# Optimization experiments

Measured on AMD Instinct MI355X. Metric: run time of the kernel, lower is better.

The kernel has to match this reference:

```python
import jax, jax.numpy as jnp
import numpy as np
from jax import lax

C = 256
K = 3
KK = K * K
PAD = 1


def conv2d(x, w, b, pad):
    # x: [B,Cin,H,W], w: [Cout,Cin,kh,kw]
    y = lax.conv_general_dilated(x, w, (1, 1), [(pad, pad), (pad, pad)],
                                 dimension_numbers=("NCHW", "OIHW", "NCHW"))
    return y + b[None, :, None, None]


def _bilinear_gather(x, ys, xs):
    # x: [B,C,H,W]; ys, xs: [B,KK,H,W] float sample coords (pixel space).
    # Zero padding outside the image (torchvision deform_conv2d semantics).
    B, Cc, H, W = x.shape
    y0 = jnp.floor(ys)
    x0 = jnp.floor(xs)
    fy = ys - y0
    fx = xs - x0
    xf = x.reshape(B, Cc, H * W)

    def gather_b(xb, ib):
        return jnp.take(xb, ib, axis=1)  # [C, KK*H*W]

    out = jnp.zeros((B, Cc, KK, H, W), dtype=x.dtype)
    corners = [
        (y0, x0, (1 - fy) * (1 - fx)),
        (y0, x0 + 1, (1 - fy) * fx),
        (y0 + 1, x0, fy * (1 - fx)),
        (y0 + 1, x0 + 1, fy * fx),
    ]
    for yi, xi, wgt in corners:
        valid = (yi >= 0) & (yi < H) & (xi >= 0) & (xi < W)
        yc = jnp.clip(yi, 0, H - 1).astype(jnp.int32)
        xc = jnp.clip(xi, 0, W - 1).astype(jnp.int32)
        idx = (yc * W + xc).reshape(B, -1)  # [B, KK*H*W]
        g = jax.vmap(gather_b)(xf, idx).reshape(B, Cc, KK, H, W)
        out = out + g * (wgt * valid.astype(x.dtype))[:, None]
    return out


def deform_conv2d(x, offset, weight):
    # x: [B,C,H,W]; offset: [B, 2*KK, H, W] with layout (k, (dy, dx));
    # weight: [Cout, Cin, K, K]; stride 1, padding 1, no mask/bias.
    B, Cin, H, W = x.shape
    off = offset.reshape(B, KK, 2, H, W)
    dy = off[:, :, 0]  # [B,KK,H,W]
    dx = off[:, :, 1]
    ky = (jnp.arange(KK, dtype=x.dtype) // K) - PAD  # kernel row offsets
    kx = (jnp.arange(KK, dtype=x.dtype) % K) - PAD
    ys = dy + jnp.arange(H, dtype=x.dtype)[None, None, :, None] + ky[None, :, None, None]
    xs = dx + jnp.arange(W, dtype=x.dtype)[None, None, None, :] + kx[None, :, None, None]
    sampled = _bilinear_gather(x, ys, xs)  # [B,Cin,KK,H,W]
    Cout = weight.shape[0]
    return jnp.einsum("bckhw,ock->bohw", sampled, weight.reshape(Cout, Cin, KK))


def setup_inputs() -> dict:
    key = jax.random.key(0)
    ks = jax.random.split(key, 12)
    B, H, W = 2, 128, 128
    s = 0.05
    inp = {
        "ft_1": jax.random.normal(ks[0], (B, C, H, W), jnp.float32),
        "ft_2": jax.random.normal(ks[1], (B, C, H, W), jnp.float32),
        "ft_3": jax.random.normal(ks[2], (B, C, H, W), jnp.float32),
        "w1": jax.random.normal(ks[3], (256, 3 * C, 3, 3), jnp.float32) * s,
        "b1": jnp.zeros((256,), jnp.float32),
        "w2": jax.random.normal(ks[4], (256, 256, 3, 3), jnp.float32) * s,
        "b2": jnp.zeros((256,), jnp.float32),
        # last offset conv is zero-init in the original; use small random
        # values so the deformable sampling path is actually exercised
        "w3": jax.random.normal(ks[5], (2 * KK * 2, 256, 3, 3), jnp.float32) * 0.01,
        "b3": jax.random.normal(ks[6], (2 * KK * 2,), jnp.float32) * 0.01,
        "w_dcn2": jax.random.normal(ks[7], (C, C, 3, 3), jnp.float32) * s,
        "w_dcn3": jax.random.normal(ks[8], (C, C, 3, 3), jnp.float32) * s,
        "w_fuse": jax.random.normal(ks[9], (C, 3 * C, 1, 1), jnp.float32) * s,
        "b_fuse": jnp.zeros((C,), jnp.float32),
    }
    return inp


def reference(ft_1, ft_2, ft_3, w1, b1, w2, b2, w3, b3,
              w_dcn2, w_dcn3, w_fuse, b_fuse):
    combined = jnp.concatenate([ft_1, ft_2, ft_3], axis=1)  # [B,3C,H,W]
    h = jax.nn.relu(conv2d(combined, w1, b1, 1))
    h = jax.nn.relu(conv2d(h, w2, b2, 1))
    offsets_all = conv2d(h, w3, b3, 1)  # [B, 36, H, W]
    half = offsets_all.shape[1] // 2
    off_2 = offsets_all[:, :half]
    off_3 = offsets_all[:, half:]
    ft_2_aligned = deform_conv2d(ft_2, off_2, w_dcn2)
    ft_3_aligned = deform_conv2d(ft_3, off_3, w_dcn3)
    fused_raw = jnp.concatenate([ft_1, ft_2_aligned, ft_3_aligned], axis=1)
    return conv2d(fused_raw, w_fuse, b_fuse, 0)
```

## Files before the change

kernel.cpp:

```cpp
#include <hip/hip_runtime.h>
#include <stdint.h>

#define H_ 128
#define W_ 128
#define HW_ 16384
#define B_ 2
#define XP_ 130

typedef __attribute__((ext_vector_type(4))) float f32x4;
typedef _Float16 half_t;
typedef __attribute__((ext_vector_type(8))) _Float16 h8v;
typedef __attribute__((ext_vector_type(4))) _Float16 h4v;

__device__ __forceinline__ f32x4 MFMA(h8v a, h8v b, f32x4 c) {
  return __builtin_amdgcn_mfma_f32_16x16x32_f16(a, b, c, 0, 0, 0);
}
__device__ __forceinline__ f32x4 zero4() {
  f32x4 z; z[0] = 0.f; z[1] = 0.f; z[2] = 0.f; z[3] = 0.f; return z;
}
__device__ __forceinline__ int swz(int r, int c8) {
  return r * 64 + ((c8 ^ (r & 7)) << 3);
}

template <int N>
__device__ __forceinline__ void s_wait_vmcnt() {
  asm volatile("s_waitcnt vmcnt(%0)" ::"n"(N) : "memory");
}

typedef const __attribute__((address_space(1))) uint32_t glb_u32;
typedef __attribute__((address_space(3))) uint32_t lds_u32;
__device__ __forceinline__ void gl_lds16(const half_t* g, half_t* l) {
  __builtin_amdgcn_global_load_lds((glb_u32*)(uintptr_t)g,
                                   (lds_u32*)(uint32_t)(uintptr_t)l, 16, 0, 0);
}

__global__ __launch_bounds__(256) void zeropad(half_t* __restrict__ buf, int C) {
  int nc = C >> 3;
  int total = B_ * 516 * nc;
  int idx = blockIdx.x * 256 + threadIdx.x;
  if (idx >= total) return;
  int c8 = idx % nc;
  int p = idx / nc;
  int b = p / 516, i = p % 516;
  int y, x;
  if (i < 130) { y = 0; x = i; }
  else if (i < 260) { y = 129; x = i - 130; }
  else if (i < 388) { y = i - 260 + 1; x = 0; }
  else { y = i - 388 + 1; x = 129; }
  h8v z;
#pragma unroll
  for (int j = 0; j < 8; ++j) z[j] = (half_t)0.f;
  *(h8v*)(buf + ((size_t)(b * XP_ + y) * XP_ + x) * C + c8 * 8) = z;
}

__global__ __launch_bounds__(256) void pack_x(
    const float* __restrict__ f1, const float* __restrict__ f2,
    const float* __restrict__ f3, half_t* __restrict__ xcat) {
  __shared__ float tile[64][65];
  int bid = blockIdx.x;
  int t = bid % 24, by = bid / 24;
  int b = by >> 7, y = by & 127;
  int s = t / 8, t2 = t % 8;
  int x0 = (t2 & 1) * 64, c0 = (t2 >> 1) * 64;
  const float* f = (s == 0) ? f1 : ((s == 1) ? f2 : f3);
  int tid = threadIdx.x;
  int rx = tid & 63, rc = tid >> 6;
  const float* srcp = f + ((size_t)(b * 256 + c0)) * HW_ + (size_t)y * W_ + x0;
#pragma unroll
  for (int i = 0; i < 16; ++i) {
    int c = rc + i * 4;
    tile[c][rx] = srcp[(size_t)c * HW_ + rx];
  }
  __syncthreads();
#pragma unroll
  for (int it = 0; it < 2; ++it) {
    int task = tid + it * 256;
    int x = task & 63, c8 = task >> 6;
    h8v v;
#pragma unroll
    for (int j = 0; j < 8; ++j) v[j] = (half_t)tile[c8 * 8 + j][x];
    size_t pix = (size_t)(b * XP_ + y + 1) * XP_ + x0 + x + 1;
    *(h8v*)(xcat + pix * 768 + s * 256 + c0 + c8 * 8) = v;
  }
}

__global__ __launch_bounds__(256) void wtrans_swz(
    const float* __restrict__ w, half_t* __restrict__ wt,
    int CO, int CI) {
  int CS = CI >> 6;
  int idx = blockIdx.x * 256 + threadIdx.x;
  int e = idx & 8191, tile = idx >> 13;
  int task = e >> 3, j = e & 7;
  int r = task >> 3, c8 = (task & 7) ^ (r & 7);
  int tpb = 9 * CS;
  int coblk = tile / tpb, within = tile - coblk * tpb;
  int dx = within % 3, q = within / 3;
  int cs = q % CS, g = q / CS;
  int t = g * 3 + dx;
  int co = coblk * 128 + r;
  int ci = cs * 64 + c8 * 8 + j;
  float v = (co < CO) ? w[((size_t)co * CI + ci) * 9 + t] : 0.f;
  wt[idx] = (half_t)v;
}

__global__ __launch_bounds__(256) void wtrans_swz256(
    const float* __restrict__ w, half_t* __restrict__ wt) {
  int idx = blockIdx.x * 256 + threadIdx.x;
  int e = idx & 16383, tile = idx >> 14;
  int task = e >> 3, j = e & 7;
  int r = task >> 3, c8 = (task & 7) ^ (r & 7);
  int cs = tile & 3, t = tile >> 2;
  int ci = cs * 64 + c8 * 8 + j;
  wt[idx] = (half_t)w[((size_t)r * 256 + ci) * 9 + t];
}

__global__ __launch_bounds__(256) void fuse_wswz(
    const float* __restrict__ w, half_t* __restrict__ wt) {
  int idx = blockIdx.x * 256 + threadIdx.x;
  int e = idx & 8191, tile = idx >> 13;
  int task = e >> 3, j = e & 7;
  int r = task >> 3, c8 = (task & 7) ^ (r & 7);
  int cs = tile % 12, coblk = tile / 12;
  int co = coblk * 128 + r;
  int ci = cs * 64 + c8 * 8 + j;
  wt[idx] = (half_t)w[(size_t)co * 768 + ci];
}

template <int CIN, bool RELU, bool FP32OUT>
__global__ __launch_bounds__(256) void conv3x3(
    const half_t* __restrict__ in, const half_t* __restrict__ wt,
    const float* __restrict__ bias, half_t* __restrict__ outb,
    float* __restrict__ outf, int COUT) {
  constexpr int CS = CIN / 64;
  constexpr int NGI = 3 * CS;
  __shared__ __align__(16) half_t wl[2][8192];
  __shared__ __align__(16) half_t al[2][8704];
  int tid = threadIdx.x;
  int by = blockIdx.x;
  int b = by >> 7, y = by & 127;
  int co0 = blockIdx.y * 128;
  int w = tid >> 6, l = tid & 63, lr = l & 15, lg = l >> 4;
  int wr = (w >> 1) * 64, wc = (w & 1) * 64;
  f32x4 acc[4][4];
#pragma unroll
  for (int i = 0; i < 4; ++i)
#pragma unroll
    for (int j = 0; j < 4; ++j) acc[i][j] = zero4();

  const half_t* wbase = wt + (size_t)blockIdx.y * (9 * CS) * 8192;

  int ldsoff[4], aoff[4], ldsoff4, aoff4;
#pragma unroll
  for (int it = 0; it < 4; ++it) {
    int task = tid + it * 256;
    ldsoff[it] = task * 8;
    int r = task >> 3, c8 = (task & 7) ^ (r & 7);
    aoff[it] = r * CIN + c8 * 8;
  }
  {
    int task = 1024 + tid;
    ldsoff4 = task * 8;
    int r = task >> 3, c8 = (task & 7) ^ (r & 7);
    aoff4 = r * CIN + c8 * 8;
  }

  auto stage_w = [&](int s, int buf) {
    const half_t* wp = wbase + (size_t)s * 8192;
#pragma unroll
    for (int it = 0; it < 4; ++it)
      gl_lds16(wp + ldsoff[it], &wl[buf][ldsoff[it]]);
  };
  auto stage_a = [&](int gi, int buf) {
    int g = gi / CS, cs = gi - g * CS;
    const half_t* ap = in + ((size_t)(b * XP_ + y + g) * XP_) * CIN + cs * 64;
    if (tid < 64) gl_lds16(ap + aoff4, &al[buf][ldsoff4]);
#pragma unroll
    for (int it = 0; it < 4; ++it)
      gl_lds16(ap + aoff[it], &al[buf][ldsoff[it]]);
  };
  auto compute = [&](int dx, int wbuf, int abuf) {
    const half_t* wb = wl[wbuf];
    const half_t* ab = al[abuf];
    h8v af[4][2], bf[4][2];
#pragma unroll
    for (int cg = 0; cg < 4; ++cg)
#pragma unroll
      for (int kc = 0; kc < 2; ++kc)
        af[cg][kc] = *(const h8v*)(wb + swz(wr + 16 * cg + lr, 4 * kc + lg));
#pragma unroll
    for (int pg = 0; pg < 4; ++pg)
#pragma unroll
      for (int kc = 0; kc < 2; ++kc)
        bf[pg][kc] = *(const h8v*)(ab + swz(wc + 16 * pg + lr + dx, 4 * kc + lg));
    __builtin_amdgcn_s_setprio(1);
#pragma unroll
    for (int cg = 0; cg < 4; ++cg)
#pragma unroll
      for (int pg = 0; pg < 4; ++pg) {
        acc[cg][pg] = MFMA(af[cg][0], bf[pg][0], acc[cg][pg]);
        acc[cg][pg] = MFMA(af[cg][1], bf[pg][1], acc[cg][pg]);
      }
    __builtin_amdgcn_s_setprio(0);
  };

  stage_w(0, 0);
  stage_a(0, 0);
  for (int gi = 0; gi < NGI; ++gi) {
    int abuf = gi & 1;
    int s0 = 3 * gi;
    stage_w(s0 + 1, (s0 + 1) & 1);
    s_wait_vmcnt<4>();
    __builtin_amdgcn_s_barrier();
    compute(0, s0 & 1, abuf);
    __builtin_amdgcn_s_barrier();
    stage_w(s0 + 2, s0 & 1);
    s_wait_vmcnt<4>();
    __builtin_amdgcn_s_barrier();
    compute(1, (s0 + 1) & 1, abuf);
    __builtin_amdgcn_s_barrier();
    if (gi + 1 < NGI) {
      stage_w(s0 + 3, (s0 + 3) & 1);
      stage_a(gi + 1, abuf ^ 1);
      s_wait_vmcnt<8>();
    } else {
      s_wait_vmcnt<0>();
    }
    __builtin_amdgcn_s_barrier();
    compute(2, s0 & 1, abuf);
    __builtin_amdgcn_s_barrier();
  }
#pragma unroll
  for (int cg = 0; cg < 4; ++cg) {
    int co = co0 + wr + 16 * cg + 4 * lg;
    if (FP32OUT && co >= COUT) continue;
    f32x4 bv = *(const f32x4*)(bias + co);
#pragma unroll
    for (int pg = 0; pg < 4; ++pg) {
      int px = wc + 16 * pg + lr;
      f32x4 v = acc[cg][pg];
#pragma unroll
      for (int r = 0; r < 4; ++r) {
        v[r] += bv[r];
        if (RELU) v[r] = fmaxf(v[r], 0.f);
      }
      if (FP32OUT) {
        size_t pix = (size_t)(b * H_ + y) * W_ + px;
        *(f32x4*)(outf + pix * COUT + co) = v;
      } else {
        size_t pix = (size_t)(b * XP_ + y + 1) * XP_ + px + 1;
        h4v pv;
#pragma unroll
        for (int r = 0; r < 4; ++r) pv[r] = (half_t)v[r];
        *(h4v*)(outb + pix * 256 + co) = pv;
      }
    }
  }
}

__global__ __launch_bounds__(512) void dcn(
    const half_t* __restrict__ xcat, int cbase,
    const float* __restrict__ off, int obase,
    const half_t* __restrict__ wt, half_t* __restrict__ outb) {
  __shared__ __align__(16) half_t wl[2][16384];
  __shared__ __align__(16) half_t al[2][8192];
  __shared__ int caddr[2][128][4];
  __shared__ float cwt[2][128][4];
  int tid = threadIdx.x;
  int bx = blockIdx.x;
  int by = ((bx & 7) << 5) | (bx >> 3);
  int b = by >> 7, y = by & 127;
  int w = tid >> 6, l = tid & 63, lr = l & 15, lg = l >> 4;
  int wr = (w >> 1) * 64, wc = (w & 1) * 64;
  size_t rowpix = (size_t)(b * H_ + y) * W_;
  f32x4 acc[4][4];
#pragma unroll
  for (int i = 0; i < 4; ++i)
#pragma unroll
    for (int j = 0; j < 4; ++j) acc[i][j] = zero4();

  auto coeffs = [&](int t) {
    if (tid < 128) {
      int px = tid;
      const float* op = off + (rowpix + px) * 36 + obase + 2 * t;
      float dy = op[0], dx = op[1];
      float ysf = (float)(y + (t / 3) - 1) + dy;
      float xsf = (float)(px + (t % 3) - 1) + dx;
      float y0f = floorf(ysf), x0f = floorf(xsf);
      float fy = ysf - y0f, fx = xsf - x0f;
      int y0 = (int)y0f, x0 = (int)x0f;
#pragma unroll
      for (int c = 0; c < 4; ++c) {
        int iy = y0 + (c >> 1), ix = x0 + (c & 1);
        float wc2 = ((c >> 1) ? fy : 1.f - fy) * ((c & 1) ? fx : 1.f - fx);
        bool valid = (iy >= 0) && (iy < H_) && (ix >= 0) && (ix < W_);
        int cy = iy < 0 ? 0 : (iy > H_ - 1 ? H_ - 1 : iy);
        int cx = ix < 0 ? 0 : (ix > W_ - 1 ? W_ - 1 : ix);
        caddr[t & 1][px][c] = ((b * XP_ + cy + 1) * XP_ + cx + 1) * 768 + cbase;
        cwt[t & 1][px][c] = valid ? wc2 : 0.f;
      }
    }
  };

  h8v cv[2][4];
  auto blendload = [&](int s) {
    int t = (s >> 2) & 1;
    int c0 = (s & 3) * 64;
#pragma unroll
    for (int it = 0; it < 2; ++it) {
      int task = tid + it * 512;
      int px = task >> 3;
      int cc = c0 + (task & 7) * 8;
#pragma unroll
      for (int c = 0; c < 4; ++c)
        cv[it][c] = *(const h8v*)(xcat + caddr[t][px][c] + cc);
    }
  };
  auto blendwrite = [&](int s, int buf) {
    int t = (s >> 2) & 1;
#pragma unroll
    for (int it = 0; it < 2; ++it) {
      int task = tid + it * 512;
      int px = task >> 3, c8 = task & 7;
      float av[8];
#pragma unroll
      for (int j = 0; j < 8; ++j) av[j] = 0.f;
#pragma unroll
      for (int c = 0; c < 4; ++c) {
        float wcf = cwt[t][px][c];
#pragma unroll
        for (int j = 0; j < 8; ++j) av[j] += wcf * (float)cv[it][c][j];
      }
      h8v pv;
#pragma unroll
      for (int j = 0; j < 8; ++j) pv[j] = (half_t)av[j];
      *(h8v*)(&al[buf][swz(px, c8)]) = pv;
    }
  };
  auto stagew = [&](int s, int buf) {
    const half_t* wp = wt + (size_t)s * 16384;
#pragma unroll
    for (int it = 0; it < 4; ++it) {
      int task = tid + it * 512;
      gl_lds16(wp + task * 8, &wl[buf][task * 8]);
    }
  };

  coeffs(0);
  __syncthreads();
  stagew(0, 0);
  blendload(0);
  blendwrite(0, 0);
  __syncthreads();
  for (int s = 0; s < 36; ++s) {
    int cur = s & 1, nxt = cur ^ 1;
    if (s + 1 < 36) {
      stagew(s + 1, nxt);
      blendload(s + 1);
    }
    if ((s & 3) == 0 && (s >> 2) + 1 < 9) coeffs((s >> 2) + 1);
    const half_t* wb = wl[cur];
    const half_t* ab = al[cur];
    h8v af[4][2], bf[4][2];
#pragma unroll
    for (int cg = 0; cg < 4; ++cg)
#pragma unroll
      for (int kc = 0; kc < 2; ++kc)
        af[cg][kc] = *(const h8v*)(wb + swz(wr + 16 * cg + lr, 4 * kc + lg));
#pragma unroll
    for (int pg = 0; pg < 4; ++pg)
#pragma unroll
      for (int kc = 0; kc < 2; ++kc)
        bf[pg][kc] = *(const h8v*)(ab + swz(wc + 16 * pg + lr, 4 * kc + lg));
    __builtin_amdgcn_s_setprio(1);
#pragma unroll
    for (int cg = 0; cg < 4; ++cg)
#pragma unroll
      for (int pg = 0; pg < 4; ++pg) {
        acc[cg][pg] = MFMA(af[cg][0], bf[pg][0], acc[cg][pg]);
        acc[cg][pg] = MFMA(af[cg][1], bf[pg][1], acc[cg][pg]);
      }
    __builtin_amdgcn_s_setprio(0);
    if (s + 1 < 36) blendwrite(s + 1, nxt);
    __syncthreads();
  }
#pragma unroll
  for (int cg = 0; cg < 4; ++cg) {
    int co = wr + 16 * cg + 4 * lg;
#pragma unroll
    for (int pg = 0; pg < 4; ++pg) {
      int px = wc + 16 * pg + lr;
      size_t pix = rowpix + px;
      f32x4 v = acc[cg][pg];
      h4v pv;
#pragma unroll
      for (int r = 0; r < 4; ++r) pv[r] = (half_t)v[r];
      *(h4v*)(outb + pix * 256 + co) = pv;
    }
  }
}

__global__ __launch_bounds__(256) void fuse1x1(
    const half_t* __restrict__ xcat, const half_t* __restrict__ al2,
    const half_t* __restrict__ al3, const half_t* __restrict__ wt,
    const float* __restrict__ bias, float* __restrict__ out) {
  __shared__ __align__(16) half_t wl[2][8192];
  __shared__ __align__(16) half_t al[2][8192];
  int tid = threadIdx.x;
  int by = blockIdx.x;
  int b = by >> 7, y = by & 127;
  int co0 = blockIdx.y * 128;
  int w = tid >> 6, l = tid & 63, lr = l & 15, lg = l >> 4;
  int pxb = (w >> 1) * 64, cob = (w & 1) * 64;
  f32x4 acc[4][4];
#pragma unroll
  for (int i = 0; i < 4; ++i)
#pragma unroll
    for (int j = 0; j < 4; ++j) acc[i][j] = zero4();

  const half_t* wbase = wt + (size_t)blockIdx.y * 12 * 8192;
  size_t rowpix = (size_t)(b * H_ + y) * W_;
  const half_t* xrow = xcat + ((size_t)(b * XP_ + y + 1) * XP_ + 1) * 768;

  int woff[4], rr[4], c8x8[4];
#pragma unroll
  for (int it = 0; it < 4; ++it) {
    int task = tid + it * 256;
    woff[it] = task * 8;
    rr[it] = task >> 3;
    c8x8[it] = (((task & 7) ^ (rr[it] & 7))) * 8;
  }

  auto stage = [&](int cs, int buf) {
    const half_t* wp = wbase + (size_t)cs * 8192;
#pragma unroll
    for (int it = 0; it < 4; ++it) gl_lds16(wp + woff[it], &wl[buf][woff[it]]);
#pragma unroll
    for (int it = 0; it < 4; ++it) {
      int kk = cs * 64 + c8x8[it];
      const half_t* sp;
      if (kk < 256) sp = xrow + (size_t)rr[it] * 768 + kk;
      else if (kk < 512) sp = al2 + (rowpix + rr[it]) * 256 + (kk - 256);
      else sp = al3 + (rowpix + rr[it]) * 256 + (kk - 512);
      gl_lds16(sp, &al[buf][woff[it]]);
    }
  };

  stage(0, 0);
  for (int cs = 0; cs < 12; ++cs) {
    int cur = cs & 1;
    if (cs + 1 < 12) {
      stage(cs + 1, cur ^ 1);
      s_wait_vmcnt<8>();
    } else {
      s_wait_vmcnt<0>();
    }
    __builtin_amdgcn_s_barrier();
    const half_t* wb = wl[cur];
    const half_t* ab = al[cur];
    h8v af[4][2], bf[4][2];
#pragma unroll
    for (int pg = 0; pg < 4; ++pg)
#pragma unroll
      for (int kc = 0; kc < 2; ++kc)
        af[pg][kc] = *(const h8v*)(ab + swz(pxb + 16 * pg + lr, 4 * kc + lg));
#pragma unroll
    for (int cg = 0; cg < 4; ++cg)
#pragma unroll
      for (int kc = 0; kc < 2; ++kc)
        bf[cg][kc] = *(const h8v*)(wb + swz(cob + 16 * cg + lr, 4 * kc + lg));
    __builtin_amdgcn_s_setprio(1);
#pragma unroll
    for (int pg = 0; pg < 4; ++pg)
#pragma unroll
      for (int cg = 0; cg < 4; ++cg) {
        acc[pg][cg] = MFMA(af[pg][0], bf[cg][0], acc[pg][cg]);
        acc[pg][cg] = MFMA(af[pg][1], bf[cg][1], acc[pg][cg]);
      }
    __builtin_amdgcn_s_setprio(0);
    __builtin_amdgcn_s_barrier();
  }
#pragma unroll
  for (int pg = 0; pg < 4; ++pg)
#pragma unroll
    for (int cg = 0; cg < 4; ++cg) {
      int px = pxb + 16 * pg + 4 * lg;
      int co = co0 + cob + 16 * cg + lr;
      float bb = bias[co];
      f32x4 v = acc[pg][cg];
#pragma unroll
      for (int r = 0; r < 4; ++r) v[r] += bb;
      *(f32x4*)(out + ((size_t)(b * 256 + co)) * HW_ + (size_t)y * W_ + px) = v;
    }
}

extern "C" void kernel_launch(void* const* d_in, const int* in_sizes, int n_in,
                              void* d_out, int out_size, void* d_ws, size_t ws_size,
                              hipStream_t stream) {
  (void)in_sizes; (void)n_in; (void)out_size; (void)ws_size;
  const float* ft1 = (const float*)d_in[0];
  const float* ft2 = (const float*)d_in[1];
  const float* ft3 = (const float*)d_in[2];
  const float* w1 = (const float*)d_in[3];
  const float* b1 = (const float*)d_in[4];
  const float* w2 = (const float*)d_in[5];
  const float* b2 = (const float*)d_in[6];
  const float* w3 = (const float*)d_in[7];
  const float* b3 = (const float*)d_in[8];
  const float* wd2 = (const float*)d_in[9];
  const float* wd3 = (const float*)d_in[10];
  const float* wf = (const float*)d_in[11];
  const float* bfu = (const float*)d_in[12];

  char* p = (char*)d_ws;
  half_t* xcat = (half_t*)p; p += (size_t)B_ * XP_ * XP_ * 768 * 2;
  half_t* h1p = (half_t*)p;  p += (size_t)B_ * XP_ * XP_ * 256 * 2;
  half_t* h2p = (half_t*)p;  p += (size_t)B_ * XP_ * XP_ * 256 * 2;
  float* off = (float*)p;    p += (size_t)B_ * HW_ * 36 * 4;
  half_t* w1t = (half_t*)p;  p += (size_t)2 * 9 * 12 * 8192 * 2;
  half_t* w2t = (half_t*)p;  p += (size_t)2 * 9 * 4 * 8192 * 2;
  half_t* w3t = (half_t*)p;  p += (size_t)1 * 9 * 4 * 8192 * 2;
  half_t* wd2t = (half_t*)p; p += (size_t)36 * 16384 * 2;
  half_t* wd3t = (half_t*)p; p += (size_t)36 * 16384 * 2;
  half_t* wft = (half_t*)p;  p += (size_t)2 * 12 * 8192 * 2;
  half_t* al2 = h1p;
  half_t* al3 = h2p;

  int zp768 = (B_ * 516 * 96 + 255) / 256;
  int zp256 = (B_ * 516 * 32 + 255) / 256;
  zeropad<<<zp768, 256, 0, stream>>>(xcat, 768);
  zeropad<<<zp256, 256, 0, stream>>>(h1p, 256);
  zeropad<<<zp256, 256, 0, stream>>>(h2p, 256);
  pack_x<<<24 * B_ * H_, 256, 0, stream>>>(ft1, ft2, ft3, xcat);
  wtrans_swz<<<6912, 256, 0, stream>>>(w1, w1t, 256, 768);
  wtrans_swz<<<2304, 256, 0, stream>>>(w2, w2t, 256, 256);
  wtrans_swz<<<1152, 256, 0, stream>>>(w3, w3t, 36, 256);
  wtrans_swz256<<<2304, 256, 0, stream>>>(wd2, wd2t);
  wtrans_swz256<<<2304, 256, 0, stream>>>(wd3, wd3t);
  fuse_wswz<<<768, 256, 0, stream>>>(wf, wft);

  conv3x3<768, true, false><<<dim3(B_ * H_, 2), 256, 0, stream>>>(xcat, w1t, b1, h1p, nullptr, 256);
  conv3x3<256, true, false><<<dim3(B_ * H_, 2), 256, 0, stream>>>(h1p, w2t, b2, h2p, nullptr, 256);
  conv3x3<256, false, true><<<dim3(B_ * H_, 1), 256, 0, stream>>>(h2p, w3t, b3, nullptr, off, 36);
  dcn<<<dim3(B_ * H_), 512, 0, stream>>>(xcat, 256, off, 0, wd2t, al2);
  dcn<<<dim3(B_ * H_), 512, 0, stream>>>(xcat, 512, off, 18, wd3t, al3);
  fuse1x1<<<dim3(B_ * H_, 2), 256, 0, stream>>>(xcat, al2, al3, wft, bfu, (float*)d_out);
}
```

Baseline: 385.9 us.

## Merge setup kernels, specialize offset conv to 64 outputs, batch DCN, fp16 blend

Merges the three zero-pad launches and six weight-transform launches into single kernels, and runs both deformable convolutions in one launch with a second grid dimension. The offset conv gets its own kernel with a 64-row output tile instead of 128, since only 36 channels are needed, which removes wasted MFMA work and weight staging. The bilinear blend now does its multiply-adds in packed fp16 with fp16 corner weights instead of fp32. This cuts launch count and arithmetic, at the cost of some precision in the blended samples.

```diff
diff --git a/kernel.cpp b/kernel.cpp
--- a/kernel.cpp
+++ b/kernel.cpp
@@ -18,6 +18,12 @@
 __device__ __forceinline__ f32x4 zero4() {
   f32x4 z; z[0] = 0.f; z[1] = 0.f; z[2] = 0.f; z[3] = 0.f; return z;
 }
+__device__ __forceinline__ h8v splat8(half_t x) {
+  h8v v;
+#pragma unroll
+  for (int j = 0; j < 8; ++j) v[j] = x;
+  return v;
+}
 __device__ __forceinline__ int swz(int r, int c8) {
   return r * 64 + ((c8 ^ (r & 7)) << 3);
 }
@@ -34,13 +40,18 @@
                                    (lds_u32*)(uint32_t)(uintptr_t)l, 16, 0, 0);
 }
 
-__global__ __launch_bounds__(256) void zeropad(half_t* __restrict__ buf, int C) {
+__global__ __launch_bounds__(256) void zeropad_all(
+    half_t* __restrict__ xcat, half_t* __restrict__ h1p,
+    half_t* __restrict__ h2p) {
+  int idx = blockIdx.x * 256 + threadIdx.x;
+  half_t* buf; int C, li;
+  if (idx < 99072) { buf = xcat; C = 768; li = idx; }
+  else if (idx < 132096) { buf = h1p; C = 256; li = idx - 99072; }
+  else if (idx < 165120) { buf = h2p; C = 256; li = idx - 132096; }
+  else return;
   int nc = C >> 3;
-  int total = B_ * 516 * nc;
-  int idx = blockIdx.x * 256 + threadIdx.x;
-  if (idx >= total) return;
-  int c8 = idx % nc;
-  int p = idx / nc;
+  int c8 = li % nc;
+  int p = li / nc;
   int b = p / 516, i = p % 516;
   int y, x;
   if (i < 130) { y = 0; x = i; }
@@ -84,11 +95,10 @@
   }
 }
 
-__global__ __launch_bounds__(256) void wtrans_swz(
-    const float* __restrict__ w, half_t* __restrict__ wt,
-    int CO, int CI) {
+__device__ __forceinline__ void wt_conv(const float* __restrict__ w,
+                                        half_t* __restrict__ wt, int CO, int CI,
+                                        int idx) {
   int CS = CI >> 6;
-  int idx = blockIdx.x * 256 + threadIdx.x;
   int e = idx & 8191, tile = idx >> 13;
   int task = e >> 3, j = e & 7;
   int r = task >> 3, c8 = (task & 7) ^ (r & 7);
@@ -102,10 +112,20 @@
   float v = (co < CO) ? w[((size_t)co * CI + ci) * 9 + t] : 0.f;
   wt[idx] = (half_t)v;
 }
-
-__global__ __launch_bounds__(256) void wtrans_swz256(
-    const float* __restrict__ w, half_t* __restrict__ wt) {
-  int idx = blockIdx.x * 256 + threadIdx.x;
+__device__ __forceinline__ void wt_c64(const float* __restrict__ w,
+                                       half_t* __restrict__ wt, int idx) {
+  int e = idx & 4095, tile = idx >> 12;
+  int task = e >> 3, j = e & 7;
+  int r = task >> 3, c8 = (task & 7) ^ (r & 7);
+  int dx = tile % 3, q = tile / 3;
+  int cs = q & 3, g = q >> 2;
+  int t = g * 3 + dx;
+  int ci = cs * 64 + c8 * 8 + j;
+  float v = (r < 36) ? w[((size_t)r * 256 + ci) * 9 + t] : 0.f;
+  wt[idx] = (half_t)v;
+}
+__device__ __forceinline__ void wt_256(const float* __restrict__ w,
+                                       half_t* __restrict__ wt, int idx) {
   int e = idx & 16383, tile = idx >> 14;
   int task = e >> 3, j = e & 7;
   int r = task >> 3, c8 = (task & 7) ^ (r & 7);
@@ -113,10 +133,8 @@
   int ci = cs * 64 + c8 * 8 + j;
   wt[idx] = (half_t)w[((size_t)r * 256 + ci) * 9 + t];
 }
-
-__global__ __launch_bounds__(256) void fuse_wswz(
-    const float* __restrict__ w, half_t* __restrict__ wt) {
-  int idx = blockIdx.x * 256 + threadIdx.x;
+__device__ __forceinline__ void wt_fuse(const float* __restrict__ w,
+                                        half_t* __restrict__ wt, int idx) {
   int e = idx & 8191, tile = idx >> 13;
   int task = e >> 3, j = e & 7;
   int r = task >> 3, c8 = (task & 7) ^ (r & 7);
@@ -126,11 +144,26 @@
   wt[idx] = (half_t)w[(size_t)co * 768 + ci];
 }
 
-template <int CIN, bool RELU, bool FP32OUT>
+__global__ __launch_bounds__(256) void wtrans_all(
+    const float* __restrict__ w1, half_t* __restrict__ w1t,
+    const float* __restrict__ w2, half_t* __restrict__ w2t,
+    const float* __restrict__ w3, half_t* __restrict__ w3t,
+    const float* __restrict__ wd2, half_t* __restrict__ wd2t,
+    const float* __restrict__ wd3, half_t* __restrict__ wd3t,
+    const float* __restrict__ wf, half_t* __restrict__ wft) {
+  int bid = blockIdx.x, tid = threadIdx.x;
+  if (bid < 6912)       wt_conv(w1, w1t, 256, 768, bid * 256 + tid);
+  else if (bid < 9216)  wt_conv(w2, w2t, 256, 256, (bid - 6912) * 256 + tid);
+  else if (bid < 9792)  wt_c64(w3, w3t, (bid - 9216) * 256 + tid);
+  else if (bid < 12096) wt_256(wd2, wd2t, (bid - 9792) * 256 + tid);
+  else if (bid < 14400) wt_256(wd3, wd3t, (bid - 12096) * 256 + tid);
+  else                  wt_fuse(wf, wft, (bid - 14400) * 256 + tid);
+}
+
+template <int CIN, bool RELU>
 __global__ __launch_bounds__(256) void conv3x3(
     const half_t* __restrict__ in, const half_t* __restrict__ wt,
-    const float* __restrict__ bias, half_t* __restrict__ outb,
-    float* __restrict__ outf, int COUT) {
+    const float* __restrict__ bias, half_t* __restrict__ outb) {
   constexpr int CS = CIN / 64;
   constexpr int NGI = 3 * CS;
   __shared__ __align__(16) half_t wl[2][8192];
@@ -232,7 +265,6 @@
 #pragma unroll
   for (int cg = 0; cg < 4; ++cg) {
     int co = co0 + wr + 16 * cg + 4 * lg;
-    if (FP32OUT && co >= COUT) continue;
     f32x4 bv = *(const f32x4*)(bias + co);
 #pragma unroll
     for (int pg = 0; pg < 4; ++pg) {
@@ -243,28 +275,145 @@
         v[r] += bv[r];
         if (RELU) v[r] = fmaxf(v[r], 0.f);
       }
-      if (FP32OUT) {
-        size_t pix = (size_t)(b * H_ + y) * W_ + px;
-        *(f32x4*)(outf + pix * COUT + co) = v;
-      } else {
-        size_t pix = (size_t)(b * XP_ + y + 1) * XP_ + px + 1;
-        h4v pv;
-#pragma unroll
-        for (int r = 0; r < 4; ++r) pv[r] = (half_t)v[r];
-        *(h4v*)(outb + pix * 256 + co) = pv;
+      size_t pix = (size_t)(b * XP_ + y + 1) * XP_ + px + 1;
+      h4v pv;
+#pragma unroll
+      for (int r = 0; r < 4; ++r) pv[r] = (half_t)v[r];
+      *(h4v*)(outb + pix * 256 + co) = pv;
+    }
+  }
+}
+
+__global__ __launch_bounds__(256) void conv3_c64(
+    const half_t* __restrict__ in, const half_t* __restrict__ wt,
+    const float* __restrict__ bias, float* __restrict__ outf) {
+  constexpr int CIN = 256, CS = 4, NGI = 12;
+  __shared__ __align__(16) half_t wl[2][4096];
+  __shared__ __align__(16) half_t al[2][8704];
+  int tid = threadIdx.x;
+  int by = blockIdx.x;
+  int b = by >> 7, y = by & 127;
+  int w = tid >> 6, l = tid & 63, lr = l & 15, lg = l >> 4;
+  int wc = w * 32;
+  f32x4 acc[4][2];
+#pragma unroll
+  for (int i = 0; i < 4; ++i)
+#pragma unroll
+    for (int j = 0; j < 2; ++j) acc[i][j] = zero4();
+
+  int ldsW[2];
+#pragma unroll
+  for (int it = 0; it < 2; ++it) ldsW[it] = (tid + it * 256) * 8;
+  int ldsoff[4], aoff[4], ldsoff4, aoff4;
+#pragma unroll
+  for (int it = 0; it < 4; ++it) {
+    int task = tid + it * 256;
+    ldsoff[it] = task * 8;
+    int r = task >> 3, c8 = (task & 7) ^ (r & 7);
+    aoff[it] = r * CIN + c8 * 8;
+  }
+  {
+    int task = 1024 + tid;
+    ldsoff4 = task * 8;
+    int r = task >> 3, c8 = (task & 7) ^ (r & 7);
+    aoff4 = r * CIN + c8 * 8;
+  }
+
+  auto stage_w = [&](int s, int buf) {
+    const half_t* wp = wt + (size_t)s * 4096;
+#pragma unroll
+    for (int it = 0; it < 2; ++it)
+      gl_lds16(wp + ldsW[it], &wl[buf][ldsW[it]]);
+  };
+  auto stage_a = [&](int gi, int buf) {
+    int g = gi / CS, cs = gi - g * CS;
+    const half_t* ap = in + ((size_t)(b * XP_ + y + g) * XP_) * CIN + cs * 64;
+    if (tid < 64) gl_lds16(ap + aoff4, &al[buf][ldsoff4]);
+#pragma unroll
+    for (int it = 0; it < 4; ++it)
+      gl_lds16(ap + aoff[it], &al[buf][ldsoff[it]]);
+  };
+  auto compute = [&](int dx, int wbuf, int abuf) {
+    const half_t* wb = wl[wbuf];
+    const half_t* ab = al[abuf];
+    h8v af[4][2], bf[2][2];
+#pragma unroll
+    for (int cg = 0; cg < 4; ++cg)
+#pragma unroll
+      for (int kc = 0; kc < 2; ++kc)
+        af[cg][kc] = *(const h8v*)(wb + swz(16 * cg + lr, 4 * kc + lg));
+#pragma unroll
+    for (int pg = 0; pg < 2; ++pg)
+#pragma unroll
+      for (int kc = 0; kc < 2; ++kc)
+        bf[pg][kc] = *(const h8v*)(ab + swz(wc + 16 * pg + lr + dx, 4 * kc + lg));
+    __builtin_amdgcn_s_setprio(1);
+#pragma unroll
+    for (int cg = 0; cg < 4; ++cg)
+#pragma unroll
+      for (int pg = 0; pg < 2; ++pg) {
+        acc[cg][pg] = MFMA(af[cg][0], bf[pg][0], acc[cg][pg]);
+        acc[cg][pg] = MFMA(af[cg][1], bf[pg][1], acc[cg][pg]);
       }
+    __builtin_amdgcn_s_setprio(0);
+  };
+
+  stage_w(0, 0);
+  stage_a(0, 0);
+  for (int gi = 0; gi < NGI; ++gi) {
+    int abuf = gi & 1;
+    int s0 = 3 * gi;
+    stage_w(s0 + 1, (s0 + 1) & 1);
+    s_wait_vmcnt<2>();
+    __builtin_amdgcn_s_barrier();
+    compute(0, s0 & 1, abuf);
+    __builtin_amdgcn_s_barrier();
+    stage_w(s0 + 2, s0 & 1);
+    s_wait_vmcnt<2>();
+    __builtin_amdgcn_s_barrier();
+    compute(1, (s0 + 1) & 1, abuf);
+    __builtin_amdgcn_s_barrier();
+    if (gi + 1 < NGI) {
+      stage_w(s0 + 3, (s0 + 3) & 1);
+      stage_a(gi + 1, abuf ^ 1);
+      s_wait_vmcnt<6>();
+    } else {
+      s_wait_vmcnt<0>();
+    }
+    __builtin_amdgcn_s_barrier();
+    compute(2, s0 & 1, abuf);
+    __builtin_amdgcn_s_barrier();
+  }
+#pragma unroll
+  for (int cg = 0; cg < 4; ++cg) {
+    int co = 16 * cg + 4 * lg;
+    if (co >= 36) continue;
+    f32x4 bv = *(const f32x4*)(bias + co);
+#pragma unroll
+    for (int pg = 0; pg < 2; ++pg) {
+      int px = wc + 16 * pg + lr;
+      f32x4 v = acc[cg][pg];
+#pragma unroll
+      for (int r = 0; r < 4; ++r) v[r] += bv[r];
+      size_t pix = (size_t)(b * H_ + y) * W_ + px;
+      *(f32x4*)(outf + pix * 36 + co) = v;
     }
   }
 }
 
 __global__ __launch_bounds__(512) void dcn(
-    const half_t* __restrict__ xcat, int cbase,
-    const float* __restrict__ off, int obase,
-    const half_t* __restrict__ wt, half_t* __restrict__ outb) {
+    const half_t* __restrict__ xcat, const float* __restrict__ off,
+    const half_t* __restrict__ wt2, const half_t* __restrict__ wt3,
+    half_t* __restrict__ out2, half_t* __restrict__ out3) {
   __shared__ __align__(16) half_t wl[2][16384];
   __shared__ __align__(16) half_t al[2][8192];
   __shared__ int caddr[2][128][4];
-  __shared__ float cwt[2][128][4];
+  __shared__ half_t chw[2][128][4];
+  int gy = blockIdx.y;
+  const half_t* wt = gy ? wt3 : wt2;
+  half_t* outb = gy ? out3 : out2;
+  int cbase = 256 + (gy << 8);
+  int obase = 18 * gy;
   int tid = threadIdx.x;
   int bx = blockIdx.x;
   int by = ((bx & 7) << 5) | (bx >> 3);
@@ -296,7 +445,7 @@
         int cy = iy < 0 ? 0 : (iy > H_ - 1 ? H_ - 1 : iy);
         int cx = ix < 0 ? 0 : (ix > W_ - 1 ? W_ - 1 : ix);
         caddr[t & 1][px][c] = ((b * XP_ + cy + 1) * XP_ + cx + 1) * 768 + cbase;
-        cwt[t & 1][px][c] = valid ? wc2 : 0.f;
+        chw[t & 1][px][c] = (half_t)(valid ? wc2 : 0.f);
       }
     }
   };
@@ -321,19 +470,11 @@
     for (int it = 0; it < 2; ++it) {
       int task = tid + it * 512;
       int px = task >> 3, c8 = task & 7;
-      float av[8];
-#pragma unroll
-      for (int j = 0; j < 8; ++j) av[j] = 0.f;
-#pragma unroll
-      for (int c = 0; c < 4; ++c) {
-        float wcf = cwt[t][px][c];
-#pragma unroll
-        for (int j = 0; j < 8; ++j) av[j] += wcf * (float)cv[it][c][j];
-      }
-      h8v pv;
-#pragma unroll
-      for (int j = 0; j < 8; ++j) pv[j] = (half_t)av[j];
-      *(h8v*)(&al[buf][swz(px, c8)]) = pv;
+      h8v av = cv[it][0] * splat8(chw[t][px][0]);
+      av += cv[it][1] * splat8(chw[t][px][1]);
+      av += cv[it][2] * splat8(chw[t][px][2]);
+      av += cv[it][3] * splat8(chw[t][px][3]);
+      *(h8v*)(&al[buf][swz(px, c8)]) = av;
     }
   };
   auto stagew = [&](int s, int buf) {
@@ -518,30 +659,21 @@
   float* off = (float*)p;    p += (size_t)B_ * HW_ * 36 * 4;
   half_t* w1t = (half_t*)p;  p += (size_t)2 * 9 * 12 * 8192 * 2;
   half_t* w2t = (half_t*)p;  p += (size_t)2 * 9 * 4 * 8192 * 2;
-  half_t* w3t = (half_t*)p;  p += (size_t)1 * 9 * 4 * 8192 * 2;
+  half_t* w3t = (half_t*)p;  p += (size_t)36 * 4096 * 2;
   half_t* wd2t = (half_t*)p; p += (size_t)36 * 16384 * 2;
   half_t* wd3t = (half_t*)p; p += (size_t)36 * 16384 * 2;
   half_t* wft = (half_t*)p;  p += (size_t)2 * 12 * 8192 * 2;
   half_t* al2 = h1p;
   half_t* al3 = h2p;
 
-  int zp768 = (B_ * 516 * 96 + 255) / 256;
-  int zp256 = (B_ * 516 * 32 + 255) / 256;
-  zeropad<<<zp768, 256, 0, stream>>>(xcat, 768);
-  zeropad<<<zp256, 256, 0, stream>>>(h1p, 256);
-  zeropad<<<zp256, 256, 0, stream>>>(h2p, 256);
+  zeropad_all<<<645, 256, 0, stream>>>(xcat, h1p, h2p);
   pack_x<<<24 * B_ * H_, 256, 0, stream>>>(ft1, ft2, ft3, xcat);
-  wtrans_swz<<<6912, 256, 0, stream>>>(w1, w1t, 256, 768);
-  wtrans_swz<<<2304, 256, 0, stream>>>(w2, w2t, 256, 256);
-  wtrans_swz<<<1152, 256, 0, stream>>>(w3, w3t, 36, 256);
-  wtrans_swz256<<<2304, 256, 0, stream>>>(wd2, wd2t);
-  wtrans_swz256<<<2304, 256, 0, stream>>>(wd3, wd3t);
-  fuse_wswz<<<768, 256, 0, stream>>>(wf, wft);
-
-  conv3x3<768, true, false><<<dim3(B_ * H_, 2), 256, 0, stream>>>(xcat, w1t, b1, h1p, nullptr, 256);
-  conv3x3<256, true, false><<<dim3(B_ * H_, 2), 256, 0, stream>>>(h1p, w2t, b2, h2p, nullptr, 256);
-  conv3x3<256, false, true><<<dim3(B_ * H_, 1), 256, 0, stream>>>(h2p, w3t, b3, nullptr, off, 36);
-  dcn<<<dim3(B_ * H_), 512, 0, stream>>>(xcat, 256, off, 0, wd2t, al2);
-  dcn<<<dim3(B_ * H_), 512, 0, stream>>>(xcat, 512, off, 18, wd3t, al3);
+  wtrans_all<<<15168, 256, 0, stream>>>(w1, w1t, w2, w2t, w3, w3t,
+                                        wd2, wd2t, wd3, wd3t, wf, wft);
+
+  conv3x3<768, true><<<dim3(B_ * H_, 2), 256, 0, stream>>>(xcat, w1t, b1, h1p);
+  conv3x3<256, true><<<dim3(B_ * H_, 2), 256, 0, stream>>>(h1p, w2t, b2, h2p);
+  conv3_c64<<<dim3(B_ * H_), 256, 0, stream>>>(h2p, w3t, b3, off);
+  dcn<<<dim3(B_ * H_, 2), 512, 0, stream>>>(xcat, off, wd2t, wd3t, al2, al3);
   fuse1x1<<<dim3(B_ * H_, 2), 256, 0, stream>>>(xcat, al2, al3, wft, bfu, (float*)d_out);
 }
```

New measurement: 332.5 us. 13.9% less time.
